# Optimization experiments

Hardware: AMD Instinct MI355X
Metric: run time of the kernel (lower is better)

## Reference

```python
import jax, jax.numpy as jnp
import numpy as np

B, T, K = 1024, 512, 64  # batch, max_seq_len, num_tags


def setup_inputs() -> dict:
    key = jax.random.key(0)
    k1, k2, k3, k4 = jax.random.split(key, 4)
    logits = jax.random.normal(k1, (B, T, K), jnp.float32)
    nwords = jax.random.randint(k2, (B,), 1, T + 1, jnp.int32)
    tags = jax.random.randint(k3, (B, T), 0, K, jnp.int32)
    limit = float(np.sqrt(6.0 / (K + K)))  # glorot_uniform for [K,K]
    crf_params = jax.random.uniform(k4, (K, K), jnp.float32, -limit, limit)
    return {"logits": logits, "nwords": nwords, "tags": tags, "crf_params": crf_params}


def _time_mask(lengths, t_len):
    # mask[t, b] = True if step (t+1) < lengths[b]  (steps 1..T-1 of the recursion)
    return (jnp.arange(1, t_len)[:, None] < lengths[None, :])


def _viterbi_decode(logits, trans, lengths):
    b, t_len, k = logits.shape
    alpha0 = logits[:, 0]                           # [B,K]
    xs = (jnp.moveaxis(logits[:, 1:], 1, 0),        # [T-1,B,K]
          _time_mask(lengths, t_len))               # [T-1,B]
    ident = jnp.arange(k)[None, :]                  # identity backpointers for padding

    def step(alpha, x):
        logit_t, m = x
        scores = alpha[:, :, None] + trans[None]    # [B,K_prev,K_cur]
        new_alpha = scores.max(axis=1) + logit_t
        bp = jnp.argmax(scores, axis=1)             # [B,K]
        m2 = m[:, None]
        return jnp.where(m2, new_alpha, alpha), jnp.where(m2, bp, ident)

    alpha, bps = jax.lax.scan(step, alpha0, xs)     # bps: [T-1,B,K]
    last = jnp.argmax(alpha, axis=-1)               # [B]

    def back(tag, bp_t):
        prev = jnp.take_along_axis(bp_t, tag[:, None], axis=1)[:, 0]
        return prev, prev

    _, prevs = jax.lax.scan(back, last, bps, reverse=True)  # prevs[t] = tag at t, t=0..T-2
    return jnp.concatenate([jnp.moveaxis(prevs, 0, 1), last[:, None]], axis=1)  # [B,T]


def _log_norm(logits, trans, lengths):
    b, t_len, k = logits.shape
    alpha0 = logits[:, 0]
    xs = (jnp.moveaxis(logits[:, 1:], 1, 0), _time_mask(lengths, t_len))

    def step(alpha, x):
        logit_t, m = x
        scores = alpha[:, :, None] + trans[None]    # [B,K_prev,K_cur]
        new_alpha = jax.nn.logsumexp(scores, axis=1) + logit_t
        return jnp.where(m[:, None], new_alpha, alpha), None

    alpha, _ = jax.lax.scan(step, alpha0, xs)
    return jax.nn.logsumexp(alpha, axis=-1)         # [B]


def _sequence_score(logits, tags, trans, lengths):
    b, t_len, _ = logits.shape
    pos = jnp.arange(t_len)
    m = (pos[None, :] < lengths[:, None]).astype(logits.dtype)            # [B,T]
    unary = jnp.sum(jnp.take_along_axis(logits, tags[..., None], axis=2)[..., 0] * m, axis=1)
    bm = (pos[None, :-1] < (lengths - 1)[:, None]).astype(logits.dtype)   # [B,T-1]
    binary = jnp.sum(trans[tags[:, :-1], tags[:, 1:]] * bm, axis=1)
    return unary + binary


def reference(logits, nwords, tags, crf_params):
    prediction_ids = _viterbi_decode(logits, crf_params, nwords)
    log_likelihood = _sequence_score(logits, tags, crf_params, nwords) - _log_norm(logits, crf_params, nwords)
    loss = jnp.mean(-log_likelihood)
    return prediction_ids, loss
```

## Files before the change

kernel.cpp:

```cpp
#include <hip/hip_runtime.h>

#define BB 1024
#define TT 512
#define KK 64

__global__ void crf_zero_loss(float* out) {
    out[(size_t)BB * TT] = 0.0f;
}

__global__ __launch_bounds__(128, 1)
void crf_fwd_kernel(const float* __restrict__ logits,
                    const int* __restrict__ nwords,
                    const int* __restrict__ tags,
                    const float* __restrict__ trans,
                    float* __restrict__ out) {
    __shared__ __align__(16) float sA[KK];
    __shared__ __align__(16) float sP[KK];
    __shared__ unsigned char sBP[TT * KK];
    __shared__ unsigned char sTag[TT];

    const int b    = blockIdx.x;
    const int tid  = threadIdx.x;
    const int lane = tid & 63;
    const int wid  = tid >> 6;
    const int len  = nwords[b];
    const float* lg = logits + (size_t)b * TT * KK;

    if (wid == 0) {
        float tc[KK];
#pragma unroll
        for (int i = 0; i < KK; ++i) tc[i] = trans[i * KK + lane];

        float alpha = lg[lane];
        sA[lane] = alpha;

        for (int t = 1; t < len; ++t) {
            float best = -__builtin_inff();
            int   bidx = 0;
#pragma unroll
            for (int q = 0; q < KK / 4; ++q) {
                const float4 a4 = reinterpret_cast<const float4*>(sA)[q];
                { float s = a4.x + tc[4*q+0]; if (s > best) { best = s; bidx = 4*q+0; } }
                { float s = a4.y + tc[4*q+1]; if (s > best) { best = s; bidx = 4*q+1; } }
                { float s = a4.z + tc[4*q+2]; if (s > best) { best = s; bidx = 4*q+2; } }
                { float s = a4.w + tc[4*q+3]; if (s > best) { best = s; bidx = 4*q+3; } }
            }
            const float logit = lg[t * KK + lane];
            alpha = best + logit;
            sBP[t * KK + lane] = (unsigned char)bidx;
            sA[lane] = alpha;
        }

        float v = alpha;
        int   idx = lane;
#pragma unroll
        for (int m = 32; m >= 1; m >>= 1) {
            const float ov = __shfl_xor(v, m);
            const int   oi = __shfl_xor(idx, m);
            if (ov > v || (ov == v && oi < idx)) { v = ov; idx = oi; }
        }
        const int last = idx;

        for (int t = len - 1 + lane; t < TT; t += 64)
            out[(size_t)b * TT + t] = (float)last;

        int tag = last;
        for (int t = len - 1; t >= 1; --t) {
            tag = sBP[t * KK + tag];
            sTag[t - 1] = (unsigned char)tag;
        }
        for (int t = lane; t < len - 1; t += 64)
            out[(size_t)b * TT + t] = (float)sTag[t];

    } else {
        float E[KK];
#pragma unroll
        for (int i = 0; i < KK; ++i) E[i] = __expf(trans[i * KK + lane]);

        float a = lg[lane];
        float C = 0.0f;
        int   tprev = tags[b * TT];
        float acc = (lane == tprev) ? a : 0.0f;

        for (int t = 1; t < len; ++t) {
            float M = a;
#pragma unroll
            for (int m = 32; m >= 1; m >>= 1) M = fmaxf(M, __shfl_xor(M, m));
            const float p = __expf(a - M);
            sP[lane] = p;

            float s0 = 0.f, s1 = 0.f, s2 = 0.f, s3 = 0.f;
#pragma unroll
            for (int q = 0; q < KK / 4; ++q) {
                const float4 p4 = reinterpret_cast<const float4*>(sP)[q];
                s0 = fmaf(p4.x, E[4*q+0], s0);
                s1 = fmaf(p4.y, E[4*q+1], s1);
                s2 = fmaf(p4.z, E[4*q+2], s2);
                s3 = fmaf(p4.w, E[4*q+3], s3);
            }
            const float sum   = (s0 + s1) + (s2 + s3);
            const float logit = lg[t * KK + lane];
            a = __logf(sum) + logit;
            C += M;

            const int tg = tags[b * TT + t];
            if (lane == tg) acc += logit;
            if (lane == 0)  acc += trans[tprev * KK + tg];
            tprev = tg;
        }

        float M = a;
#pragma unroll
        for (int m = 32; m >= 1; m >>= 1) M = fmaxf(M, __shfl_xor(M, m));
        float e = __expf(a - M);
#pragma unroll
        for (int m = 32; m >= 1; m >>= 1) e += __shfl_xor(e, m);
        const float log_norm = C + M + __logf(e);

#pragma unroll
        for (int m = 32; m >= 1; m >>= 1) acc += __shfl_xor(acc, m);

        if (lane == 0)
            atomicAdd(out + (size_t)BB * TT, (log_norm - acc) * (1.0f / BB));
    }
}

extern "C" void kernel_launch(void* const* d_in, const int* in_sizes, int n_in,
                              void* d_out, int out_size, void* d_ws, size_t ws_size,
                              hipStream_t stream) {
    const float* logits = (const float*)d_in[0];
    const int*   nwords = (const int*)d_in[1];
    const int*   tags   = (const int*)d_in[2];
    const float* trans  = (const float*)d_in[3];
    float*       out    = (float*)d_out;

    crf_zero_loss<<<1, 1, 0, stream>>>(out);
    crf_fwd_kernel<<<BB, 128, 0, stream>>>(logits, nwords, tags, trans, out);
}
```

Measured before the change: 543.0 us.

## Sort sequences by length for load balance and split K across half-waves

```diff
diff --git a/kernel.cpp b/kernel.cpp
--- a/kernel.cpp
+++ b/kernel.cpp
@@ -4,62 +4,139 @@
 #define TT 512
 #define KK 64
 
-__global__ void crf_zero_loss(float* out) {
-    out[(size_t)BB * TT] = 0.0f;
+__global__ void crf_setup(const int* __restrict__ nwords,
+                          int* __restrict__ rank2batch,
+                          float* __restrict__ out) {
+    __shared__ int hist[TT];
+    const int tid = threadIdx.x;
+    if (tid < TT) hist[tid] = 0;
+    __syncthreads();
+    for (int b = tid; b < BB; b += 512)
+        atomicAdd(&hist[TT - nwords[b]], 1);
+    __syncthreads();
+    if (tid == 0) {
+        int run = 0;
+        for (int k = 0; k < TT; ++k) { int c = hist[k]; hist[k] = run; run += c; }
+        out[(size_t)BB * TT] = 0.0f;
+    }
+    __syncthreads();
+    for (int b = tid; b < BB; b += 512) {
+        int r = atomicAdd(&hist[TT - nwords[b]], 1);
+        rank2batch[r] = b;
+    }
 }
+
+#define COMB(v, i, v2, i2)                                   \
+    { bool _t = ((v2) > (v)) || ((v2) == (v) && (i2) < (i)); \
+      (v) = _t ? (v2) : (v); (i) = _t ? (i2) : (i); }
 
 __global__ __launch_bounds__(128, 1)
 void crf_fwd_kernel(const float* __restrict__ logits,
                     const int* __restrict__ nwords,
                     const int* __restrict__ tags,
                     const float* __restrict__ trans,
+                    const int* __restrict__ rank2batch,
                     float* __restrict__ out) {
     __shared__ __align__(16) float sA[KK];
     __shared__ __align__(16) float sP[KK];
     __shared__ unsigned char sBP[TT * KK];
     __shared__ unsigned char sTag[TT];
 
-    const int b    = blockIdx.x;
+    const int bid  = blockIdx.x;
+    const int cu   = bid & 255, slot = bid >> 8;
+    const int r    = (slot == 0) ? cu : (slot == 1) ? (511 - cu)
+                   : (slot == 2) ? (512 + cu) : (1023 - cu);
+    const int b    = rank2batch[r];
+
     const int tid  = threadIdx.x;
     const int lane = tid & 63;
     const int wid  = tid >> 6;
+    const int m    = lane & 31;
+    const int h    = lane >> 5;
     const int len  = nwords[b];
-    const float* lg = logits + (size_t)b * TT * KK;
+    const float*  lg  = logits + (size_t)b * TT * KK;
+    const float2* lg2 = (const float2*)lg;
+    const float2* tr2 = (const float2*)trans;
 
     if (wid == 0) {
-        float tc[KK];
-#pragma unroll
-        for (int i = 0; i < KK; ++i) tc[i] = trans[i * KK + lane];
-
-        float alpha = lg[lane];
-        sA[lane] = alpha;
-
+        float tA[32], tB[32];
+#pragma unroll
+        for (int i = 0; i < 32; ++i) {
+            float2 t2 = tr2[(32 * h + i) * 32 + m];
+            tA[i] = t2.x; tB[i] = t2.y;
+        }
+
+        float2 lgt = lg2[m];
+        float a0 = lgt.x, a1 = lgt.y;
+        if (h == 0) ((float2*)sA)[m] = make_float2(a0, a1);
+
+        float2 lgt_nxt = lg2[32 * min(1, len - 1) + m];
         for (int t = 1; t < len; ++t) {
-            float best = -__builtin_inff();
-            int   bidx = 0;
-#pragma unroll
-            for (int q = 0; q < KK / 4; ++q) {
-                const float4 a4 = reinterpret_cast<const float4*>(sA)[q];
-                { float s = a4.x + tc[4*q+0]; if (s > best) { best = s; bidx = 4*q+0; } }
-                { float s = a4.y + tc[4*q+1]; if (s > best) { best = s; bidx = 4*q+1; } }
-                { float s = a4.z + tc[4*q+2]; if (s > best) { best = s; bidx = 4*q+2; } }
-                { float s = a4.w + tc[4*q+3]; if (s > best) { best = s; bidx = 4*q+3; } }
-            }
-            const float logit = lg[t * KK + lane];
-            alpha = best + logit;
-            sBP[t * KK + lane] = (unsigned char)bidx;
-            sA[lane] = alpha;
-        }
-
-        float v = alpha;
-        int   idx = lane;
-#pragma unroll
-        for (int m = 32; m >= 1; m >>= 1) {
-            const float ov = __shfl_xor(v, m);
-            const int   oi = __shfl_xor(idx, m);
-            if (ov > v || (ov == v && oi < idx)) { v = ov; idx = oi; }
-        }
-        const int last = idx;
+            lgt = lgt_nxt;
+            lgt_nxt = lg2[32 * min(t + 1, len - 1) + m];
+
+            float4 a4[8];
+#pragma unroll
+            for (int q = 0; q < 8; ++q) a4[q] = ((const float4*)sA)[h * 8 + q];
+
+            float bx, by, bz, bw; int ix, iy, iz, iw;
+            {
+                int base = 32 * h;
+                bx = a4[0].x + tA[0]; ix = base;
+                by = a4[0].y + tA[1]; iy = base + 1;
+                bz = a4[0].z + tA[2]; iz = base + 2;
+                bw = a4[0].w + tA[3]; iw = base + 3;
+#pragma unroll
+                for (int q = 1; q < 8; ++q) {
+                    int ib = base + 4 * q;
+                    float sx = a4[q].x + tA[4*q+0]; if (sx > bx) { bx = sx; ix = ib; }
+                    float sy = a4[q].y + tA[4*q+1]; if (sy > by) { by = sy; iy = ib+1; }
+                    float sz = a4[q].z + tA[4*q+2]; if (sz > bz) { bz = sz; iz = ib+2; }
+                    float sw = a4[q].w + tA[4*q+3]; if (sw > bw) { bw = sw; iw = ib+3; }
+                }
+                COMB(bx, ix, by, iy); COMB(bx, ix, bz, iz); COMB(bx, ix, bw, iw);
+            }
+            float pv0 = __shfl_xor(bx, 32); int pi0 = __shfl_xor(ix, 32);
+            COMB(bx, ix, pv0, pi0);
+            a0 = bx + lgt.x;
+            int bp0 = ix;
+
+            {
+                int base = 32 * h;
+                bx = a4[0].x + tB[0]; ix = base;
+                by = a4[0].y + tB[1]; iy = base + 1;
+                bz = a4[0].z + tB[2]; iz = base + 2;
+                bw = a4[0].w + tB[3]; iw = base + 3;
+#pragma unroll
+                for (int q = 1; q < 8; ++q) {
+                    int ib = base + 4 * q;
+                    float sx = a4[q].x + tB[4*q+0]; if (sx > bx) { bx = sx; ix = ib; }
+                    float sy = a4[q].y + tB[4*q+1]; if (sy > by) { by = sy; iy = ib+1; }
+                    float sz = a4[q].z + tB[4*q+2]; if (sz > bz) { bz = sz; iz = ib+2; }
+                    float sw = a4[q].w + tB[4*q+3]; if (sw > bw) { bw = sw; iw = ib+3; }
+                }
+                COMB(bx, ix, by, iy); COMB(bx, ix, bz, iz); COMB(bx, ix, bw, iw);
+            }
+            float pv1 = __shfl_xor(bx, 32); int pi1 = __shfl_xor(ix, 32);
+            COMB(bx, ix, pv1, pi1);
+            a1 = bx + lgt.y;
+            int bp1 = ix;
+
+            if (h == 0) {
+                ((unsigned short*)sBP)[t * 32 + m] =
+                    (unsigned short)((bp0 & 0xff) | ((bp1 & 0xff) << 8));
+                ((float2*)sA)[m] = make_float2(a0, a1);
+            }
+        }
+
+        float bv = a0; int bj = 2 * m;
+        { float v2 = a1; int i2 = 2 * m + 1; COMB(bv, bj, v2, i2); }
+#pragma unroll
+        for (int msk = 1; msk <= 16; msk <<= 1) {
+            float ov = __shfl_xor(bv, msk); int oj = __shfl_xor(bj, msk);
+            COMB(bv, bj, ov, oj);
+        }
+        const int last = bj;
 
         for (int t = len - 1 + lane; t < TT; t += 64)
             out[(size_t)b * TT + t] = (float)last;
@@ -73,52 +150,68 @@
             out[(size_t)b * TT + t] = (float)sTag[t];
 
     } else {
-        float E[KK];
-#pragma unroll
-        for (int i = 0; i < KK; ++i) E[i] = __expf(trans[i * KK + lane]);
-
-        float a = lg[lane];
+        float eA[32], eB[32];
+#pragma unroll
+        for (int i = 0; i < 32; ++i) {
+            float2 t2 = tr2[(32 * h + i) * 32 + m];
+            eA[i] = __expf(t2.x); eB[i] = __expf(t2.y);
+        }
+
+        float2 lgt = lg2[m];
+        float a0 = lgt.x, a1 = lgt.y;
         float C = 0.0f;
-        int   tprev = tags[b * TT];
-        float acc = (lane == tprev) ? a : 0.0f;
-
+        int tg = tags[b * TT];
+        float acc = 0.0f;
+        if (h == 0) { if (tg == 2*m) acc = lgt.x; else if (tg == 2*m+1) acc = lgt.y; }
+        int tprev = tg;
+
+        float2 lgt_nxt = lg2[32 * min(1, len - 1) + m];
         for (int t = 1; t < len; ++t) {
-            float M = a;
-#pragma unroll
-            for (int m = 32; m >= 1; m >>= 1) M = fmaxf(M, __shfl_xor(M, m));
-            const float p = __expf(a - M);
-            sP[lane] = p;
-
-            float s0 = 0.f, s1 = 0.f, s2 = 0.f, s3 = 0.f;
-#pragma unroll
-            for (int q = 0; q < KK / 4; ++q) {
-                const float4 p4 = reinterpret_cast<const float4*>(sP)[q];
-                s0 = fmaf(p4.x, E[4*q+0], s0);
-                s1 = fmaf(p4.y, E[4*q+1], s1);
-                s2 = fmaf(p4.z, E[4*q+2], s2);
-                s3 = fmaf(p4.w, E[4*q+3], s3);
-            }
-            const float sum   = (s0 + s1) + (s2 + s3);
-            const float logit = lg[t * KK + lane];
-            a = __logf(sum) + logit;
+            lgt = lgt_nxt;
+            lgt_nxt = lg2[32 * min(t + 1, len - 1) + m];
+
+            float M = fmaxf(a0, a1);
+#pragma unroll
+            for (int msk = 1; msk <= 16; msk <<= 1) M = fmaxf(M, __shfl_xor(M, msk));
+
+            float p0 = __expf(a0 - M), p1 = __expf(a1 - M);
+            if (h == 0) ((float2*)sP)[m] = make_float2(p0, p1);
+
+            float sx0 = 0.f, sy0 = 0.f, sz0 = 0.f, sw0 = 0.f;
+            float sx1 = 0.f, sy1 = 0.f, sz1 = 0.f, sw1 = 0.f;
+#pragma unroll
+            for (int q = 0; q < 8; ++q) {
+                float4 p4 = ((const float4*)sP)[h * 8 + q];
+                sx0 = fmaf(p4.x, eA[4*q+0], sx0); sy0 = fmaf(p4.y, eA[4*q+1], sy0);
+                sz0 = fmaf(p4.z, eA[4*q+2], sz0); sw0 = fmaf(p4.w, eA[4*q+3], sw0);
+                sx1 = fmaf(p4.x, eB[4*q+0], sx1); sy1 = fmaf(p4.y, eB[4*q+1], sy1);
+                sz1 = fmaf(p4.z, eB[4*q+2], sz1); sw1 = fmaf(p4.w, eB[4*q+3], sw1);
+            }
+            float S0 = (sx0 + sy0) + (sz0 + sw0);
+            float S1 = (sx1 + sy1) + (sz1 + sw1);
+            S0 += __shfl_xor(S0, 32);
+            S1 += __shfl_xor(S1, 32);
+
+            a0 = __logf(S0) + lgt.x;
+            a1 = __logf(S1) + lgt.y;
             C += M;
 
-            const int tg = tags[b * TT + t];
-            if (lane == tg) acc += logit;
-            if (lane == 0)  acc += trans[tprev * KK + tg];
+            tg = tags[b * TT + t];
+            if (h == 0) { if (tg == 2*m) acc += lgt.x; else if (tg == 2*m+1) acc += lgt.y; }
+            if (lane == 0) acc += trans[tprev * KK + tg];
             tprev = tg;
         }
 
-        float M = a;
-#pragma unroll
-        for (int m = 32; m >= 1; m >>= 1) M = fmaxf(M, __shfl_xor(M, m));
-        float e = __expf(a - M);
-#pragma unroll
-        for (int m = 32; m >= 1; m >>= 1) e += __shfl_xor(e, m);
-        const float log_norm = C + M + __logf(e);
-
-#pragma unroll
-        for (int m = 32; m >= 1; m >>= 1) acc += __shfl_xor(acc, m);
+        float Mf = fmaxf(a0, a1);
+#pragma unroll
+        for (int msk = 1; msk <= 16; msk <<= 1) Mf = fmaxf(Mf, __shfl_xor(Mf, msk));
+        float e = __expf(a0 - Mf) + __expf(a1 - Mf);
+#pragma unroll
+        for (int msk = 1; msk <= 16; msk <<= 1) e += __shfl_xor(e, msk);
+        const float log_norm = C + Mf + __logf(e);
+
+#pragma unroll
+        for (int msk = 1; msk <= 32; msk <<= 1) acc += __shfl_xor(acc, msk);
 
         if (lane == 0)
             atomicAdd(out + (size_t)BB * TT, (log_norm - acc) * (1.0f / BB));
@@ -133,7 +226,8 @@
     const int*   tags   = (const int*)d_in[2];
     const float* trans  = (const float*)d_in[3];
     float*       out    = (float*)d_out;
-
-    crf_zero_loss<<<1, 1, 0, stream>>>(out);
-    crf_fwd_kernel<<<BB, 128, 0, stream>>>(logits, nwords, tags, trans, out);
+    int*         rank2batch = (int*)d_ws;
+
+    crf_setup<<<1, 512, 0, stream>>>(nwords, rank2batch, out);
+    crf_fwd_kernel<<<BB, 128, 0, stream>>>(logits, nwords, tags, trans, rank2batch, out);
 }
```

Result: slower. 697.7 us (+28.5%).

## Sort sequences by length for load balancing; rescale forward pass lazily in linear space

Applied to the files above, without the earlier changes.

```diff
diff --git a/kernel.cpp b/kernel.cpp
--- a/kernel.cpp
+++ b/kernel.cpp
@@ -4,25 +4,57 @@
 #define TT 512
 #define KK 64
 
-__global__ void crf_zero_loss(float* out) {
-    out[(size_t)BB * TT] = 0.0f;
+__global__ void crf_setup(const int* __restrict__ nwords,
+                          int* __restrict__ rank2batch,
+                          float* __restrict__ out) {
+    __shared__ int hist[TT];
+    const int tid = threadIdx.x;
+    for (int k = tid; k < TT; k += 256) hist[k] = 0;
+    __syncthreads();
+    for (int b = tid; b < BB; b += 256) atomicAdd(&hist[TT - nwords[b]], 1);
+    __syncthreads();
+    if (tid < 64) {
+        int s = 0;
+#pragma unroll
+        for (int k = 0; k < 8; ++k) s += hist[tid * 8 + k];
+        int incl = s;
+        for (int d = 1; d < 64; d <<= 1) { int o = __shfl_up(incl, d); if (tid >= d) incl += o; }
+        int run = incl - s;
+#pragma unroll
+        for (int k = 0; k < 8; ++k) { int c = hist[tid * 8 + k]; hist[tid * 8 + k] = run; run += c; }
+    }
+    if (tid == 0) out[(size_t)BB * TT] = 0.0f;
+    __syncthreads();
+    for (int b = tid; b < BB; b += 256) {
+        int r = atomicAdd(&hist[TT - nwords[b]], 1);
+        rank2batch[r] = b;
+    }
 }
+
+#define COMB(v, i, v2, i2)                                   \
+    { bool _t = ((v2) > (v)) || ((v2) == (v) && (i2) < (i)); \
+      (v) = _t ? (v2) : (v); (i) = _t ? (i2) : (i); }
 
 __global__ __launch_bounds__(128, 1)
 void crf_fwd_kernel(const float* __restrict__ logits,
                     const int* __restrict__ nwords,
                     const int* __restrict__ tags,
                     const float* __restrict__ trans,
+                    const int* __restrict__ rank2batch,
                     float* __restrict__ out) {
     __shared__ __align__(16) float sA[KK];
-    __shared__ __align__(16) float sP[KK];
+    __shared__ __align__(16) float sU[KK];
     __shared__ unsigned char sBP[TT * KK];
     __shared__ unsigned char sTag[TT];
 
-    const int b    = blockIdx.x;
-    const int tid  = threadIdx.x;
-    const int lane = tid & 63;
-    const int wid  = tid >> 6;
+    const int bid  = blockIdx.x;
+    const int cu   = bid & 255, slot = bid >> 8;
+    const int r    = (slot == 0) ? cu : (slot == 1) ? (511 - cu)
+                   : (slot == 2) ? (512 + cu) : (1023 - cu);
+    const int b    = rank2batch[r];
+
+    const int lane = threadIdx.x & 63;
+    const int wid  = threadIdx.x >> 6;
     const int len  = nwords[b];
     const float* lg = logits + (size_t)b * TT * KK;
 
@@ -34,30 +66,40 @@
         float alpha = lg[lane];
         sA[lane] = alpha;
 
+        float f1 = lg[(len > 1 ? 1 : 0) * KK + lane];
+        float f2 = lg[(len > 2 ? 2 : (len - 1)) * KK + lane];
+
         for (int t = 1; t < len; ++t) {
-            float best = -__builtin_inff();
-            int   bidx = 0;
+            const float logit = f1;
+            f1 = f2;
+            int tn = t + 2; if (tn > len - 1) tn = len - 1;
+            f2 = lg[tn * KK + lane];
+
+            float4 aq = ((const float4*)sA)[0];
+            float bx = aq.x + tc[0]; int ix = 0;
+            float by = aq.y + tc[1]; int iy = 1;
+            float bz = aq.z + tc[2]; int iz = 2;
+            float bw = aq.w + tc[3]; int iw = 3;
 #pragma unroll
-            for (int q = 0; q < KK / 4; ++q) {
-                const float4 a4 = reinterpret_cast<const float4*>(sA)[q];
-                { float s = a4.x + tc[4*q+0]; if (s > best) { best = s; bidx = 4*q+0; } }
-                { float s = a4.y + tc[4*q+1]; if (s > best) { best = s; bidx = 4*q+1; } }
-                { float s = a4.z + tc[4*q+2]; if (s > best) { best = s; bidx = 4*q+2; } }
-                { float s = a4.w + tc[4*q+3]; if (s > best) { best = s; bidx = 4*q+3; } }
+            for (int q = 1; q < 16; ++q) {
+                float4 a4 = ((const float4*)sA)[q];
+                float sx = a4.x + tc[4*q+0]; if (sx > bx) { bx = sx; ix = 4*q+0; }
+                float sy = a4.y + tc[4*q+1]; if (sy > by) { by = sy; iy = 4*q+1; }
+                float sz = a4.z + tc[4*q+2]; if (sz > bz) { bz = sz; iz = 4*q+2; }
+                float sw = a4.w + tc[4*q+3]; if (sw > bw) { bw = sw; iw = 4*q+3; }
             }
-            const float logit = lg[t * KK + lane];
-            alpha = best + logit;
-            sBP[t * KK + lane] = (unsigned char)bidx;
+            COMB(bx, ix, by, iy); COMB(bz, iz, bw, iw); COMB(bx, ix, bz, iz);
+
+            alpha = bx + logit;
+            sBP[t * KK + lane] = (unsigned char)ix;
             sA[lane] = alpha;
         }
 
-        float v = alpha;
-        int   idx = lane;
+        float v = alpha; int idx = lane;
 #pragma unroll
         for (int m = 32; m >= 1; m >>= 1) {
-            const float ov = __shfl_xor(v, m);
-            const int   oi = __shfl_xor(idx, m);
-            if (ov > v || (ov == v && oi < idx)) { v = ov; idx = oi; }
+            float ov = __shfl_xor(v, m); int oi = __shfl_xor(idx, m);
+            COMB(v, idx, ov, oi);
         }
         const int last = idx;
 
@@ -77,45 +119,61 @@
 #pragma unroll
         for (int i = 0; i < KK; ++i) E[i] = __expf(trans[i * KK + lane]);
 
-        float a = lg[lane];
-        float C = 0.0f;
-        int   tprev = tags[b * TT];
-        float acc = (lane == tprev) ? a : 0.0f;
+        const float lg0 = lg[lane];
+        float M = lg0;
+#pragma unroll
+        for (int m = 32; m >= 1; m >>= 1) M = fmaxf(M, __shfl_xor(M, m));
+        float C = M;
+        float u = __expf(lg0 - M);
+        sU[lane] = u;
+
+        int tprev = tags[b * TT];
+        float acc = (lane == tprev) ? lg0 : 0.0f;
+
+        float f1 = lg[(len > 1 ? 1 : 0) * KK + lane];
+        float f2 = lg[(len > 2 ? 2 : (len - 1)) * KK + lane];
+        int tg1 = tags[b * TT + (len > 1 ? 1 : 0)];
+        int tg2 = tags[b * TT + (len > 2 ? 2 : (len - 1))];
 
         for (int t = 1; t < len; ++t) {
-            float M = a;
-#pragma unroll
-            for (int m = 32; m >= 1; m >>= 1) M = fmaxf(M, __shfl_xor(M, m));
-            const float p = __expf(a - M);
-            sP[lane] = p;
+            const float logit = f1; f1 = f2;
+            const int tg = tg1; tg1 = tg2;
+            int tn = t + 2; if (tn > len - 1) tn = len - 1;
+            f2  = lg[tn * KK + lane];
+            tg2 = tags[b * TT + tn];
 
             float s0 = 0.f, s1 = 0.f, s2 = 0.f, s3 = 0.f;
 #pragma unroll
-            for (int q = 0; q < KK / 4; ++q) {
-                const float4 p4 = reinterpret_cast<const float4*>(sP)[q];
-                s0 = fmaf(p4.x, E[4*q+0], s0);
-                s1 = fmaf(p4.y, E[4*q+1], s1);
-                s2 = fmaf(p4.z, E[4*q+2], s2);
-                s3 = fmaf(p4.w, E[4*q+3], s3);
+            for (int q = 0; q < 16; ++q) {
+                float4 u4 = ((const float4*)sU)[q];
+                s0 = fmaf(u4.x, E[4*q+0], s0);
+                s1 = fmaf(u4.y, E[4*q+1], s1);
+                s2 = fmaf(u4.z, E[4*q+2], s2);
+                s3 = fmaf(u4.w, E[4*q+3], s3);
             }
-            const float sum   = (s0 + s1) + (s2 + s3);
-            const float logit = lg[t * KK + lane];
-            a = __logf(sum) + logit;
-            C += M;
+            u = ((s0 + s1) + (s2 + s3)) * __expf(logit);
 
-            const int tg = tags[b * TT + t];
+            if ((t & 7) == 0) {
+                float mx = u;
+#pragma unroll
+                for (int m = 32; m >= 1; m >>= 1) mx = fmaxf(mx, __shfl_xor(mx, m));
+                u *= (1.0f / mx);
+                C += __logf(mx);
+            }
+            sU[lane] = u;
+
             if (lane == tg) acc += logit;
             if (lane == 0)  acc += trans[tprev * KK + tg];
             tprev = tg;
         }
 
-        float M = a;
+        float mx = u;
 #pragma unroll
-        for (int m = 32; m >= 1; m >>= 1) M = fmaxf(M, __shfl_xor(M, m));
-        float e = __expf(a - M);
+        for (int m = 32; m >= 1; m >>= 1) mx = fmaxf(mx, __shfl_xor(mx, m));
+        float e = u * (1.0f / mx);
 #pragma unroll
         for (int m = 32; m >= 1; m >>= 1) e += __shfl_xor(e, m);
-        const float log_norm = C + M + __logf(e);
+        const float log_norm = C + __logf(mx) + __logf(e);
 
 #pragma unroll
         for (int m = 32; m >= 1; m >>= 1) acc += __shfl_xor(acc, m);
@@ -133,7 +191,8 @@
     const int*   tags   = (const int*)d_in[2];
     const float* trans  = (const float*)d_in[3];
     float*       out    = (float*)d_out;
+    int*         rank2batch = (int*)d_ws;
 
-    crf_zero_loss<<<1, 1, 0, stream>>>(out);
-    crf_fwd_kernel<<<BB, 128, 0, stream>>>(logits, nwords, tags, trans, out);
+    crf_setup<<<1, 256, 0, stream>>>(nwords, rank2batch, out);
+    crf_fwd_kernel<<<BB, 128, 0, stream>>>(logits, nwords, tags, trans, rank2batch, out);
 }
```

Measured after the change: 651.1 us. 1.2x slower.
